# Optimization experiments

Hardware: AMD Instinct MI355X
Metric: run time of the kernel (lower is better)

The kernel has to match this reference:

```python
import jax, jax.numpy as jnp
import numpy as np
from functools import lru_cache
from jax.scipy.linalg import expm

N_QUBITS = 6
DIM = 2 ** N_QUBITS          # 64
N_PAULI = 4 ** N_QUBITS      # 4096


@lru_cache(maxsize=None)
def _pauli_tensor_np(n_qubits):
    # All n-qubit Pauli strings as dense matrices, ordered base-4
    # (digit 0..3 -> I, X, Y, Z; most-significant digit = first qubit).
    I = np.eye(2, dtype=np.complex64)
    X = np.array([[0, 1], [1, 0]], dtype=np.complex64)
    Y = np.array([[0, -1j], [1j, 0]], dtype=np.complex64)
    Z = np.array([[1, 0], [0, -1]], dtype=np.complex64)
    base = np.stack([I, X, Y, Z])  # [4,2,2]
    T = base
    for _ in range(n_qubits - 1):
        k, d = T.shape[0], T.shape[1]
        T = np.einsum('iab,jcd->ijacbd', T, base).reshape(k * 4, d * 2, d * 2)
    return np.ascontiguousarray(T.astype(np.complex64))  # [4^n, 2^n, 2^n]


def setup_inputs() -> dict:
    key = jax.random.key(0)
    kx, kw, kb = jax.random.split(key, 3)
    x = jax.random.normal(kx, (512, 4000), dtype=jnp.float32)
    weight = jax.random.normal(kw, (4, N_PAULI - 1), dtype=jnp.float32)
    bias = jax.random.normal(kb, (DIM,), dtype=jnp.float32)
    return {"x": x, "weight": weight, "bias": bias}


def reference(x, weight, bias):
    # x: [B, in_dim] float32; weight: [n_reps, 4^n - 1]; bias: [out_dim]
    B, in_dim = x.shape
    n_reps = weight.shape[0]
    out_dim = bias.shape[0]
    P = jnp.asarray(_pauli_tensor_np(N_QUBITS))  # [4096, 64, 64] complex64

    # Pad data coefficients up to the full Pauli basis (identity included).
    xp = jnp.pad(x, ((0, 0), (0, N_PAULI - in_dim))).astype(jnp.complex64)

    # Data-encoding Hamiltonian per sample: H_d[b] = sum_p x[b,p] * P[p]
    Hd = jnp.einsum('bp,pij->bij', xp, P)                       # [B,64,64]
    Ud = jax.vmap(expm)(-1j * Hd)                               # [B,64,64]

    # Trainable Hamiltonians per rep (identity Pauli excluded -> global phase).
    Hp = jnp.einsum('rp,pij->rij', weight.astype(jnp.complex64), P[1:])
    Up = jax.vmap(expm)(-1j * Hp)                               # [R,64,64]

    # Data re-uploading circuit on |0...0>: repeat (U_param @ U_data).
    psi = jnp.zeros((B, DIM), dtype=jnp.complex64).at[:, 0].set(1.0)
    for r in range(n_reps):
        psi = jnp.einsum('bij,bj->bi', Ud, psi)
        psi = jnp.einsum('ij,bj->bi', Up[r], psi)

    # Observables are computational-basis projectors |k><k|, k < out_dim:
    # <psi|O_k|psi> = |psi_k|^2
    probs = (psi[:, :out_dim].real ** 2 + psi[:, :out_dim].imag ** 2)
    return probs.astype(jnp.float32) + bias
```

## Files before the change

kernel.cpp:

```cpp
#include <hip/hip_runtime.h>
#include <math.h>

typedef float2 cplx;
typedef __attribute__((ext_vector_type(8))) short short8v;
typedef __attribute__((ext_vector_type(4))) short short4v;
typedef __attribute__((ext_vector_type(4))) float float4v;

#define IN_DIM 4000
#define NREPS 4

#define C0f  1.0f
#define C1f  1.0f
#define C2f  0.5f
#define C3f  0.16666667f
#define C4f  0.041666668f
#define C5f  8.3333333e-3f
#define C6f  1.3888889e-3f
#define C7f  1.9841270e-4f
#define C8f  2.4801587e-5f
#define C9f  2.7557319e-6f
#define C10f 2.7557319e-7f
#define C11f 2.5052108e-8f
#define C12f 2.0876757e-9f
#define C13f 1.6059044e-10f
#define C14f 1.1470746e-11f
#define C15f 7.6471637e-13f

#define MFMA(A,B,C) __builtin_amdgcn_mfma_f32_16x16x32_bf16((A),(B),(C),0,0,0)


__device__ __forceinline__ int idxSw(int a, int b) {
    return (a << 6) + ((((b >> 3) + a) & 7) << 3) + (b & 7);
}
__device__ __forceinline__ short f2bf(float f) {
    unsigned u = __float_as_uint(f);
    return (short)((u + 0x7FFF + ((u >> 16) & 1)) >> 16);
}
__device__ __forceinline__ float bf2f(short s) {
    return __uint_as_float(((unsigned)(unsigned short)s) << 16);
}
__device__ __forceinline__ short8v neg8(short8v a) {
    int4 u; __builtin_memcpy(&u, &a, 16);
    u.x ^= 0x80008000; u.y ^= 0x80008000; u.z ^= 0x80008000; u.w ^= 0x80008000;
    short8v r; __builtin_memcpy(&r, &u, 16); return r;
}

template<int AM, int BM, int NDM, int NDN>
__device__ __forceinline__ void mm_mfma(const short* __restrict__ As,
                                        const short* __restrict__ Bs,
                                        int li, int q, int mb, int nb,
                                        float4v* __restrict__ accR,
                                        float4v* __restrict__ accI)
{
    #pragma unroll
    for (int ks = 0; ks < 2; ks++) {
        const int ch = ks * 4 + q;
        short8v arh[NDM], arl[NDM], cRh[NDM], cRl[NDM], cIh[NDM], cIl[NDM];
        #pragma unroll
        for (int dm = 0; dm < NDM; dm++) {
            int r = ((mb + dm) << 4) + li;
            int off = (r << 6) + (((ch + r) & 7) << 3);
            arh[dm] = *(const short8v*)(As + off);
            arl[dm] = *(const short8v*)(As + 4096 + off);
            short8v aih = *(const short8v*)(As + 8192 + off);
            short8v ail = *(const short8v*)(As + 12288 + off);
            short8v nih = neg8(aih), nil_ = neg8(ail);
            cRh[dm] = (AM == 2) ? aih : nih;
            cRl[dm] = (AM == 2) ? ail : nil_;
            cIh[dm] = (AM == 2) ? nih : aih;
            cIl[dm] = (AM == 2) ? nil_ : ail;
        }
        #pragma unroll
        for (int dn = 0; dn < NDN; dn++) {
            int n = ((nb + dn) << 4) + li;
            int off = (n << 6) + (((ch + n) & 7) << 3);
            short8v brh = *(const short8v*)(Bs + off);
            short8v brl = *(const short8v*)(Bs + 4096 + off);
            short8v bih = *(const short8v*)(Bs + 8192 + off);
            short8v bil = *(const short8v*)(Bs + 12288 + off);
            if (BM == 1) { brh = neg8(brh); brl = neg8(brl); }
            __builtin_amdgcn_s_setprio(1);
            #pragma unroll
            for (int dm = 0; dm < NDM; dm++) {
                int ti = dm * NDN + dn;
                accR[ti] = MFMA(arh[dm], brh, accR[ti]);
                accR[ti] = MFMA(arh[dm], brl, accR[ti]);
                accR[ti] = MFMA(arl[dm], brh, accR[ti]);
                accR[ti] = MFMA(cRh[dm], bih, accR[ti]);
                accR[ti] = MFMA(cRh[dm], bil, accR[ti]);
                accR[ti] = MFMA(cRl[dm], bih, accR[ti]);
                accI[ti] = MFMA(arh[dm], bih, accI[ti]);
                accI[ti] = MFMA(arh[dm], bil, accI[ti]);
                accI[ti] = MFMA(arl[dm], bih, accI[ti]);
                accI[ti] = MFMA(cIh[dm], brh, accI[ti]);
                accI[ti] = MFMA(cIh[dm], brl, accI[ti]);
                accI[ti] = MFMA(cIl[dm], brh, accI[ti]);
            }
            __builtin_amdgcn_s_setprio(0);
        }
    }
}

template<int NDM, int NDN>
__device__ __forceinline__ void write_row(short* __restrict__ S, int li, int q,
                                          int mb, int nb,
                                          const float4v* cre, const float4v* cim)
{
    #pragma unroll
    for (int dm = 0; dm < NDM; dm++)
    #pragma unroll
    for (int dn = 0; dn < NDN; dn++) {
        int ti = dm * NDN + dn;
        int c = ((nb + dn) << 4) + li;
        #pragma unroll
        for (int reg = 0; reg < 4; reg++) {
            int r = ((mb + dm) << 4) + q * 4 + reg;
            int off = idxSw(r, c);
            float vr = cre[ti][reg], vi = cim[ti][reg];
            short rh = f2bf(vr), rl = f2bf(vr - bf2f(rh));
            short ih = f2bf(vi), il = f2bf(vi - bf2f(ih));
            S[off] = rh; S[4096 + off] = rl; S[8192 + off] = ih; S[12288 + off] = il;
        }
    }
}

template<int NDM, int NDN>
__device__ __forceinline__ void write_rowT(short* __restrict__ S, int li, int q,
                                           int mb, int nb,
                                           const float4v* cre, const float4v* cim)
{
    #pragma unroll
    for (int dm = 0; dm < NDM; dm++)
    #pragma unroll
    for (int dn = 0; dn < NDN; dn++) {
        int ti = dm * NDN + dn;
        int c = ((nb + dn) << 4) + li;
        int k0 = ((mb + dm) << 4) + q * 4;
        int off = idxSw(c, k0);
        short4v rh, rl, ih, il;
        #pragma unroll
        for (int reg = 0; reg < 4; reg++) {
            float vr = cre[ti][reg], vi = cim[ti][reg];
            short h1 = f2bf(vr); rh[reg] = h1; rl[reg] = f2bf(vr - bf2f(h1));
            short h2 = f2bf(vi); ih[reg] = h2; il[reg] = f2bf(vi - bf2f(h2));
        }
        *(short4v*)(S + off) = rh;
        *(short4v*)(S + 4096 + off) = rl;
        *(short4v*)(S + 8192 + off) = ih;
        *(short4v*)(S + 12288 + off) = il;
    }
}

template<int NDM, int NDN>
__device__ __forceinline__ void gather_tile(const short* __restrict__ S, int li, int q,
                                            int mb, int nb, float4v* bre, float4v* bim)
{
    #pragma unroll
    for (int dm = 0; dm < NDM; dm++)
    #pragma unroll
    for (int dn = 0; dn < NDN; dn++) {
        int ti = dm * NDN + dn;
        int c = ((nb + dn) << 4) + li;
        #pragma unroll
        for (int reg = 0; reg < 4; reg++) {
            int r = ((mb + dm) << 4) + q * 4 + reg;
            int off = idxSw(r, c);
            bre[ti][reg] = bf2f(S[off]) + bf2f(S[4096 + off]);
            bim[ti][reg] = bf2f(S[8192 + off]) + bf2f(S[12288 + off]);
        }
    }
}

template<int NDM, int NDN>
__device__ __forceinline__ void adddiag(float4v* u, float cI, int li, int q, int mb, int nb)
{
    #pragma unroll
    for (int dm = 0; dm < NDM; dm++)
    #pragma unroll
    for (int dn = 0; dn < NDN; dn++) {
        if (mb + dm == nb + dn) {
            #pragma unroll
            for (int e = 0; e < 4; e++)
                if (li == q * 4 + e) u[dm * NDN + dn][e] += cI;
        }
    }
}

template<int NDM, int NDN>
__device__ __forceinline__ void store_tiles(cplx* __restrict__ dst, int li, int q,
                                            int mb, int nb,
                                            const float4v* ure, const float4v* uim)
{
    #pragma unroll
    for (int dm = 0; dm < NDM; dm++)
    #pragma unroll
    for (int dn = 0; dn < NDN; dn++) {
        int ti = dm * NDN + dn;
        int c = ((nb + dn) << 4) + li;
        int cs = c ^ (((c >> 4) & 1) << 1);
        #pragma unroll
        for (int reg = 0; reg < 4; reg++) {
            int r = ((mb + dm) << 4) + q * 4 + reg;
            dst[(r << 6) + cs] = make_float2(ure[ti][reg], uim[ti][reg]);
        }
    }
}

__device__ __forceinline__ cplx pauli_phase(float v, int xm, int zm) {
    int ny = __popc(xm & zm) & 3;
    if (ny == 0) return make_float2(v, 0.f);
    if (ny == 1) return make_float2(0.f, -v);
    if (ny == 2) return make_float2(-v, 0.f);
    return make_float2(0.f, v);
}

__device__ __forceinline__ void expm_core8(char* __restrict__ LDS,
                                           const float* __restrict__ src, bool isW,
                                           int t, float4v* ure, float4v* uim)
{
    constexpr int NDM = 1, NDN = 2, NT = 2;
    short* S0 = (short*)LDS;
    short* S1 = (short*)(LDS + 32768);
    cplx*  W  = (cplx*)(LDS + 32768);
    float* red = (float*)(LDS + 65536);
    const int lane = t & 63, wv = t >> 6;
    const int li = lane & 15, q = lane >> 4;
    const int mb = wv & 3, nb = (wv >> 2) << 1;

    float sumsq = 0.f;
    #pragma unroll
    for (int n = 0; n < 8; n++) {
        int p = t + 512 * n;
        int xm = 0, zm = 0;
        #pragma unroll
        for (int k = 0; k < 6; k++) {
            int d = (p >> (2 * k)) & 3;
            int hi = d >> 1, lo = d & 1;
            zm |= hi << k; xm |= (hi ^ lo) << k;
        }
        float v = isW ? ((p == 0) ? 0.f : src[p - 1])
                      : ((p < IN_DIM) ? src[p] : 0.f);
        sumsq += v * v;
        W[(xm << 6) + zm] = pauli_phase(v, xm, zm);
    }
    #pragma unroll
    for (int d = 32; d >= 1; d >>= 1) sumsq += __shfl_xor(sumsq, d, 64);
    if (lane == 0) red[wv] = sumsq;
    __syncthreads();

    float rs = 0.f;
    #pragma unroll
    for (int i2 = 0; i2 < 8; i2++) rs += red[i2];
    float fro = sqrtf(64.f * rs);
    int s1 = 0; { float nn = fro; while (nn > 8.f && s1 < 24) { nn *= 0.5f; s1++; } }
    float sc1 = exp2f((float)(-s1));

    cplx hv[8];
    #pragma unroll
    for (int rr = 0; rr < 8; rr++) hv[rr] = W[((wv * 8 + rr) << 6) + lane];
    #pragma unroll
    for (int d = 1; d < 64; d <<= 1) {
        float sg = (lane & d) ? -1.f : 1.f;
        #pragma unroll
        for (int rr = 0; rr < 8; rr++) {
            float px = __shfl_xor(hv[rr].x, d, 64);
            float py = __shfl_xor(hv[rr].y, d, 64);
            hv[rr].x = fmaf(sg, hv[rr].x, px);
            hv[rr].y = fmaf(sg, hv[rr].y, py);
        }
    }

    #pragma unroll
    for (int rr = 0; rr < 8; rr++) {
        int m = wv * 8 + rr;
        int c = lane ^ m;
        float vr = hv[rr].y * sc1, vi = -hv[rr].x * sc1;
        short rh = f2bf(vr), rl = f2bf(vr - bf2f(rh));
        short ih = f2bf(vi), il = f2bf(vi - bf2f(ih));
        int off = idxSw(lane, c);
        S0[off] = rh; S0[4096 + off] = rl; S0[8192 + off] = ih; S0[12288 + off] = il;
    }
    __syncthreads();

    const float4v z4 = {0.f, 0.f, 0.f, 0.f};
    float4v accR[NT], accI[NT];
    #define ZERO_ACC _Pragma("unroll") for (int i2 = 0; i2 < NT; i2++) { accR[i2]=z4; accI[i2]=z4; }

    ZERO_ACC
    mm_mfma<0, 1, NDM, NDN>(S0, S0, li, q, mb, nb, accR, accI);
    float ss = 0.f;
    #pragma unroll
    for (int ti = 0; ti < NT; ti++)
        #pragma unroll
        for (int e = 0; e < 4; e++)
            ss += accR[ti][e]*accR[ti][e] + accI[ti][e]*accI[ti][e];
    #pragma unroll
    for (int d = 32; d >= 1; d >>= 1) ss += __shfl_xor(ss, d, 64);
    if (lane == 0) red[8 + wv] = ss;
    __syncthreads();

    rs = 0.f;
    #pragma unroll
    for (int i2 = 0; i2 < 8; i2++) rs += red[8 + i2];
    float bound = sqrtf(sqrtf(rs));
    int ds = 0; { float nn = bound; while (nn > 3.4f && ds < 12) { nn *= 0.5f; ds++; } }
    const int s = s1 + ds;
    float dsc = exp2f((float)(-ds)), dsc2 = dsc * dsc;

    float4v bre[NT], bim[NT];
    gather_tile<NDM, NDN>(S0, li, q, mb, nb, bre, bim);

    #pragma unroll
    for (int ti = 0; ti < NT; ti++) { ure[ti] = accR[ti] * dsc2; uim[ti] = accI[ti] * dsc2; }
    write_rowT<NDM, NDN>(S1, li, q, mb, nb, ure, uim);
    __syncthreads();

    {
        float ca = C15f * dsc;
        #pragma unroll
        for (int ti = 0; ti < NT; ti++) { ure[ti] = ca * bre[ti]; uim[ti] = ca * bim[ti]; }
        adddiag<NDM, NDN>(ure, C14f, li, q, mb, nb);
        write_rowT<NDM, NDN>(S0, li, q, mb, nb, ure, uim);
    }
    __syncthreads();

    const float cIc[7] = { C0f, C2f, C4f, C6f, C8f, C10f, C12f };
    const float cAc[7] = { C1f, C3f, C5f, C7f, C9f, C11f, C13f };
    for (int j = 6; j >= 0; j--) {
        ZERO_ACC
        mm_mfma<2, 0, NDM, NDN>(S1, S0, li, q, mb, nb, accR, accI);
        __syncthreads();
        float ca = cAc[j] * dsc, cI = cIc[j];
        #pragma unroll
        for (int ti = 0; ti < NT; ti++) {
            ure[ti] = accR[ti] + ca * bre[ti];
            uim[ti] = accI[ti] + ca * bim[ti];
        }
        adddiag<NDM, NDN>(ure, cI, li, q, mb, nb);
        write_rowT<NDM, NDN>(S0, li, q, mb, nb, ure, uim);
        __syncthreads();
    }

    for (int sq = 0; sq < s; sq++) {
        write_row<NDM, NDN>(S1, li, q, mb, nb, ure, uim);
        if (sq > 0) write_rowT<NDM, NDN>(S0, li, q, mb, nb, ure, uim);
        __syncthreads();
        ZERO_ACC
        mm_mfma<0, 0, NDM, NDN>(S1, S0, li, q, mb, nb, accR, accI);
        __syncthreads();
        #pragma unroll
        for (int ti = 0; ti < NT; ti++) { ure[ti] = accR[ti]; uim[ti] = accI[ti]; }
    }
    #undef ZERO_ACC
}

__device__ __forceinline__ cplx matvec_wave8(const cplx* __restrict__ M,
                                             const cplx* __restrict__ pin,
                                             int lane, int wv)
{
    const int ri = lane & 7;
    const int rr = (wv << 3) + ri;
    const int kc = lane >> 3;
    const int ch = (kc + ri) & 7;
    const int b  = (ch >> 1) & 1;
    const float4* Mr = (const float4*)(M + (rr << 6)) + (ch << 2);
    float4 m0 = Mr[0 ^ b], m1 = Mr[1 ^ b], m2 = Mr[2 ^ b], m3 = Mr[3 ^ b];
    const cplx* p = pin + (ch << 3);
    cplx p0 = p[0], p1 = p[1], p2 = p[2], p3 = p[3];
    cplx p4 = p[4], p5 = p[5], p6 = p[6], p7 = p[7];
    float ax = 0.f, ay = 0.f;
    ax = fmaf(m0.x, p0.x, fmaf(-m0.y, p0.y, ax));
    ay = fmaf(m0.x, p0.y, fmaf( m0.y, p0.x, ay));
    ax = fmaf(m0.z, p1.x, fmaf(-m0.w, p1.y, ax));
    ay = fmaf(m0.z, p1.y, fmaf( m0.w, p1.x, ay));
    ax = fmaf(m1.x, p2.x, fmaf(-m1.y, p2.y, ax));
    ay = fmaf(m1.x, p2.y, fmaf( m1.y, p2.x, ay));
    ax = fmaf(m1.z, p3.x, fmaf(-m1.w, p3.y, ax));
    ay = fmaf(m1.z, p3.y, fmaf( m1.w, p3.x, ay));
    ax = fmaf(m2.x, p4.x, fmaf(-m2.y, p4.y, ax));
    ay = fmaf(m2.x, p4.y, fmaf( m2.y, p4.x, ay));
    ax = fmaf(m2.z, p5.x, fmaf(-m2.w, p5.y, ax));
    ay = fmaf(m2.z, p5.y, fmaf( m2.w, p5.x, ay));
    ax = fmaf(m3.x, p6.x, fmaf(-m3.y, p6.y, ax));
    ay = fmaf(m3.x, p6.y, fmaf( m3.y, p6.x, ay));
    ax = fmaf(m3.z, p7.x, fmaf(-m3.w, p7.y, ax));
    ay = fmaf(m3.z, p7.y, fmaf( m3.w, p7.x, ay));
    ax += __shfl_xor(ax, 8, 64);  ay += __shfl_xor(ay, 8, 64);
    ax += __shfl_xor(ax, 16, 64); ay += __shfl_xor(ay, 16, 64);
    ax += __shfl_xor(ax, 32, 64); ay += __shfl_xor(ay, 32, 64);
    return make_float2(ax, ay);
}

__global__ __launch_bounds__(512, 2) void circuit_kernel(const float* __restrict__ x,
                                                         const float* __restrict__ w,
                                                         const float* __restrict__ bias,
                                                         cplx* __restrict__ ws,
                                                         int* __restrict__ flag,
                                                         float* __restrict__ out)
{
    __shared__ float4 LDSf4[4168];
    char* LDS = (char*)LDSf4;
    const int t = threadIdx.x, b = blockIdx.x;
    const int lane = t & 63, wv = t >> 6, li = lane & 15, q = lane >> 4;
    const int mb = wv & 3, nb = (wv >> 2) << 1;
    float4v ure[2], uim[2];

    for (int duty = (b < NREPS) ? 0 : 1; duty < 2; duty++) {
        const bool isW = (duty == 0);
        const float* src = isW ? (w + (size_t)b * 4095) : (x + (size_t)b * IN_DIM);
        expm_core8(LDS, src, isW, t, ure, uim);
        if (isW) {
            store_tiles<1, 2>(ws + ((size_t)b << 12), li, q, mb, nb, ure, uim);
            __syncthreads();
            if (t == 0)
                __hip_atomic_fetch_add(flag, 1, __ATOMIC_RELEASE, __HIP_MEMORY_SCOPE_AGENT);
        }
    }

    cplx* Ud   = (cplx*)(LDS + 32768);
    cplx* UpS  = (cplx*)LDS;
    cplx* psiA = (cplx*)(LDS + 65664);
    cplx* psiB = (cplx*)(LDS + 66176);

    store_tiles<1, 2>(Ud, li, q, mb, nb, ure, uim);
    if (t < 64) psiA[t] = make_float2(t == 0 ? 1.f : 0.f, 0.f);
    if (t == 0) {
        while (__hip_atomic_load(flag, __ATOMIC_ACQUIRE, __HIP_MEMORY_SCOPE_AGENT) < NREPS)
            __builtin_amdgcn_s_sleep(8);
    }
    __syncthreads();

    const int rowi = (wv << 3) + (lane & 7);
    for (int r = 0; r < NREPS; r++) {
        {
            const float4* srcv = (const float4*)(ws + ((size_t)r << 12));
            float4* dstY = (float4*)UpS;
            #pragma unroll
            for (int n = 0; n < 4; n++) dstY[n * 512 + t] = srcv[n * 512 + t];
        }
        cplx v1 = matvec_wave8(Ud, psiA, lane, wv);
        if (lane < 8) psiB[rowi] = v1;
        __syncthreads();
        cplx v2 = matvec_wave8(UpS, psiB, lane, wv);
        if (lane < 8) psiA[rowi] = v2;
        __syncthreads();
    }
    if (t < 64) {
        cplx pv = psiA[t];
        out[(b << 6) + t] = fmaf(pv.x, pv.x, fmaf(pv.y, pv.y, bias[t]));
    }
}

extern "C" void kernel_launch(void* const* d_in, const int* in_sizes, int n_in,
                              void* d_out, int out_size, void* d_ws, size_t ws_size,
                              hipStream_t stream)
{
    const float* x    = (const float*)d_in[0];
    const float* w    = (const float*)d_in[1];
    const float* bias = (const float*)d_in[2];
    float* out = (float*)d_out;
    cplx* ws   = (cplx*)d_ws;
    int* flag  = (int*)((char*)d_ws + (NREPS << 15));

    int B = in_sizes[0] / IN_DIM;

    hipMemsetAsync(flag, 0, sizeof(int), stream);
    hipLaunchKernelGGL(circuit_kernel, dim3(B), dim3(512), 0, stream,
                       x, w, bias, ws, flag, out);
}
```

Measured before the change: 175.2 us.

## Use 1024-thread blocks with one MFMA tile per wave and double-buffered LDS

Doubles the block to 16 waves so each wave computes a single 16x16 complex tile instead of two, and grows LDS to 128KB with four split-bf16 buffers. The Horner loop ping-pongs between two buffers to drop one barrier per step, and squaring alternates buffer pairs. The matvec is re-partitioned across 16 waves. In exchange, only one block fits per CU (previously two of 512 threads), and the larger LDS footprint lowers occupancy across the 512 independent blocks.

```diff
diff --git a/kernel.cpp b/kernel.cpp
--- a/kernel.cpp
+++ b/kernel.cpp
@@ -45,7 +45,7 @@
     short8v r; __builtin_memcpy(&r, &u, 16); return r;
 }
 
-template<int AM, int BM, int NDM, int NDN>
+template<int AM, int BM>
 __device__ __forceinline__ void mm_mfma(const short* __restrict__ As,
                                         const short* __restrict__ Bs,
                                         int li, int q, int mb, int nb,
@@ -55,154 +55,109 @@
     #pragma unroll
     for (int ks = 0; ks < 2; ks++) {
         const int ch = ks * 4 + q;
-        short8v arh[NDM], arl[NDM], cRh[NDM], cRl[NDM], cIh[NDM], cIl[NDM];
-        #pragma unroll
-        for (int dm = 0; dm < NDM; dm++) {
-            int r = ((mb + dm) << 4) + li;
-            int off = (r << 6) + (((ch + r) & 7) << 3);
-            arh[dm] = *(const short8v*)(As + off);
-            arl[dm] = *(const short8v*)(As + 4096 + off);
-            short8v aih = *(const short8v*)(As + 8192 + off);
-            short8v ail = *(const short8v*)(As + 12288 + off);
-            short8v nih = neg8(aih), nil_ = neg8(ail);
-            cRh[dm] = (AM == 2) ? aih : nih;
-            cRl[dm] = (AM == 2) ? ail : nil_;
-            cIh[dm] = (AM == 2) ? nih : aih;
-            cIl[dm] = (AM == 2) ? nil_ : ail;
-        }
-        #pragma unroll
-        for (int dn = 0; dn < NDN; dn++) {
-            int n = ((nb + dn) << 4) + li;
-            int off = (n << 6) + (((ch + n) & 7) << 3);
-            short8v brh = *(const short8v*)(Bs + off);
-            short8v brl = *(const short8v*)(Bs + 4096 + off);
-            short8v bih = *(const short8v*)(Bs + 8192 + off);
-            short8v bil = *(const short8v*)(Bs + 12288 + off);
-            if (BM == 1) { brh = neg8(brh); brl = neg8(brl); }
-            __builtin_amdgcn_s_setprio(1);
-            #pragma unroll
-            for (int dm = 0; dm < NDM; dm++) {
-                int ti = dm * NDN + dn;
-                accR[ti] = MFMA(arh[dm], brh, accR[ti]);
-                accR[ti] = MFMA(arh[dm], brl, accR[ti]);
-                accR[ti] = MFMA(arl[dm], brh, accR[ti]);
-                accR[ti] = MFMA(cRh[dm], bih, accR[ti]);
-                accR[ti] = MFMA(cRh[dm], bil, accR[ti]);
-                accR[ti] = MFMA(cRl[dm], bih, accR[ti]);
-                accI[ti] = MFMA(arh[dm], bih, accI[ti]);
-                accI[ti] = MFMA(arh[dm], bil, accI[ti]);
-                accI[ti] = MFMA(arl[dm], bih, accI[ti]);
-                accI[ti] = MFMA(cIh[dm], brh, accI[ti]);
-                accI[ti] = MFMA(cIh[dm], brl, accI[ti]);
-                accI[ti] = MFMA(cIl[dm], brh, accI[ti]);
-            }
-            __builtin_amdgcn_s_setprio(0);
-        }
-    }
-}
-
-template<int NDM, int NDN>
-__device__ __forceinline__ void write_row(short* __restrict__ S, int li, int q,
-                                          int mb, int nb,
-                                          const float4v* cre, const float4v* cim)
-{
-    #pragma unroll
-    for (int dm = 0; dm < NDM; dm++)
-    #pragma unroll
-    for (int dn = 0; dn < NDN; dn++) {
-        int ti = dm * NDN + dn;
-        int c = ((nb + dn) << 4) + li;
-        #pragma unroll
-        for (int reg = 0; reg < 4; reg++) {
-            int r = ((mb + dm) << 4) + q * 4 + reg;
-            int off = idxSw(r, c);
-            float vr = cre[ti][reg], vi = cim[ti][reg];
-            short rh = f2bf(vr), rl = f2bf(vr - bf2f(rh));
-            short ih = f2bf(vi), il = f2bf(vi - bf2f(ih));
-            S[off] = rh; S[4096 + off] = rl; S[8192 + off] = ih; S[12288 + off] = il;
-        }
-    }
-}
-
-template<int NDM, int NDN>
-__device__ __forceinline__ void write_rowT(short* __restrict__ S, int li, int q,
+        int r = (mb << 4) + li;
+        int offA = (r << 6) + (((ch + r) & 7) << 3);
+        short8v arh = *(const short8v*)(As + offA);
+        short8v arl = *(const short8v*)(As + 4096 + offA);
+        short8v aih = *(const short8v*)(As + 8192 + offA);
+        short8v ail = *(const short8v*)(As + 12288 + offA);
+        short8v nih = neg8(aih), nil_ = neg8(ail);
+        short8v cRh = (AM == 2) ? aih : nih;
+        short8v cRl = (AM == 2) ? ail : nil_;
+        short8v cIh = (AM == 2) ? nih : aih;
+        short8v cIl = (AM == 2) ? nil_ : ail;
+
+        int n = (nb << 4) + li;
+        int offB = (n << 6) + (((ch + n) & 7) << 3);
+        short8v brh = *(const short8v*)(Bs + offB);
+        short8v brl = *(const short8v*)(Bs + 4096 + offB);
+        short8v bih = *(const short8v*)(Bs + 8192 + offB);
+        short8v bil = *(const short8v*)(Bs + 12288 + offB);
+        if (BM == 1) { brh = neg8(brh); brl = neg8(brl); }
+
+        accR[0] = MFMA(arh, brh, accR[0]);
+        accR[0] = MFMA(arh, brl, accR[0]);
+        accR[0] = MFMA(arl, brh, accR[0]);
+        accR[0] = MFMA(cRh, bih, accR[0]);
+        accR[0] = MFMA(cRh, bil, accR[0]);
+        accR[0] = MFMA(cRl, bih, accR[0]);
+        accI[0] = MFMA(arh, bih, accI[0]);
+        accI[0] = MFMA(arh, bil, accI[0]);
+        accI[0] = MFMA(arl, bih, accI[0]);
+        accI[0] = MFMA(cIh, brh, accI[0]);
+        accI[0] = MFMA(cIh, brl, accI[0]);
+        accI[0] = MFMA(cIl, brh, accI[0]);
+    }
+}
+
+__device__ __forceinline__ void write_row1(short* __restrict__ S, int li, int q,
                                            int mb, int nb,
                                            const float4v* cre, const float4v* cim)
 {
-    #pragma unroll
-    for (int dm = 0; dm < NDM; dm++)
-    #pragma unroll
-    for (int dn = 0; dn < NDN; dn++) {
-        int ti = dm * NDN + dn;
-        int c = ((nb + dn) << 4) + li;
-        int k0 = ((mb + dm) << 4) + q * 4;
-        int off = idxSw(c, k0);
-        short4v rh, rl, ih, il;
+    int c = (nb << 4) + li;
+    #pragma unroll
+    for (int reg = 0; reg < 4; reg++) {
+        int r = (mb << 4) + q * 4 + reg;
+        int off = idxSw(r, c);
+        float vr = cre[0][reg], vi = cim[0][reg];
+        short rh = f2bf(vr), rl = f2bf(vr - bf2f(rh));
+        short ih = f2bf(vi), il = f2bf(vi - bf2f(ih));
+        S[off] = rh; S[4096 + off] = rl; S[8192 + off] = ih; S[12288 + off] = il;
+    }
+}
+
+__device__ __forceinline__ void write_rowT1(short* __restrict__ S, int li, int q,
+                                            int mb, int nb,
+                                            const float4v* cre, const float4v* cim)
+{
+    int c = (nb << 4) + li;
+    int k0 = (mb << 4) + q * 4;
+    int off = idxSw(c, k0);
+    short4v rh, rl, ih, il;
+    #pragma unroll
+    for (int reg = 0; reg < 4; reg++) {
+        float vr = cre[0][reg], vi = cim[0][reg];
+        short h1 = f2bf(vr); rh[reg] = h1; rl[reg] = f2bf(vr - bf2f(h1));
+        short h2 = f2bf(vi); ih[reg] = h2; il[reg] = f2bf(vi - bf2f(h2));
+    }
+    *(short4v*)(S + off) = rh;
+    *(short4v*)(S + 4096 + off) = rl;
+    *(short4v*)(S + 8192 + off) = ih;
+    *(short4v*)(S + 12288 + off) = il;
+}
+
+__device__ __forceinline__ void gather_tile1(const short* __restrict__ S, int li, int q,
+                                             int mb, int nb, float4v* bre, float4v* bim)
+{
+    int c = (nb << 4) + li;
+    #pragma unroll
+    for (int reg = 0; reg < 4; reg++) {
+        int r = (mb << 4) + q * 4 + reg;
+        int off = idxSw(r, c);
+        bre[0][reg] = bf2f(S[off]) + bf2f(S[4096 + off]);
+        bim[0][reg] = bf2f(S[8192 + off]) + bf2f(S[12288 + off]);
+    }
+}
+
+__device__ __forceinline__ void adddiag1(float4v* u, float cI, int li, int q, int mb, int nb)
+{
+    if (mb == nb) {
         #pragma unroll
-        for (int reg = 0; reg < 4; reg++) {
-            float vr = cre[ti][reg], vi = cim[ti][reg];
-            short h1 = f2bf(vr); rh[reg] = h1; rl[reg] = f2bf(vr - bf2f(h1));
-            short h2 = f2bf(vi); ih[reg] = h2; il[reg] = f2bf(vi - bf2f(h2));
-        }
-        *(short4v*)(S + off) = rh;
-        *(short4v*)(S + 4096 + off) = rl;
-        *(short4v*)(S + 8192 + off) = ih;
-        *(short4v*)(S + 12288 + off) = il;
-    }
-}
-
-template<int NDM, int NDN>
-__device__ __forceinline__ void gather_tile(const short* __restrict__ S, int li, int q,
-                                            int mb, int nb, float4v* bre, float4v* bim)
-{
-    #pragma unroll
-    for (int dm = 0; dm < NDM; dm++)
-    #pragma unroll
-    for (int dn = 0; dn < NDN; dn++) {
-        int ti = dm * NDN + dn;
-        int c = ((nb + dn) << 4) + li;
-        #pragma unroll
-        for (int reg = 0; reg < 4; reg++) {
-            int r = ((mb + dm) << 4) + q * 4 + reg;
-            int off = idxSw(r, c);
-            bre[ti][reg] = bf2f(S[off]) + bf2f(S[4096 + off]);
-            bim[ti][reg] = bf2f(S[8192 + off]) + bf2f(S[12288 + off]);
-        }
-    }
-}
-
-template<int NDM, int NDN>
-__device__ __forceinline__ void adddiag(float4v* u, float cI, int li, int q, int mb, int nb)
-{
-    #pragma unroll
-    for (int dm = 0; dm < NDM; dm++)
-    #pragma unroll
-    for (int dn = 0; dn < NDN; dn++) {
-        if (mb + dm == nb + dn) {
-            #pragma unroll
-            for (int e = 0; e < 4; e++)
-                if (li == q * 4 + e) u[dm * NDN + dn][e] += cI;
-        }
-    }
-}
-
-template<int NDM, int NDN>
-__device__ __forceinline__ void store_tiles(cplx* __restrict__ dst, int li, int q,
-                                            int mb, int nb,
-                                            const float4v* ure, const float4v* uim)
-{
-    #pragma unroll
-    for (int dm = 0; dm < NDM; dm++)
-    #pragma unroll
-    for (int dn = 0; dn < NDN; dn++) {
-        int ti = dm * NDN + dn;
-        int c = ((nb + dn) << 4) + li;
-        int cs = c ^ (((c >> 4) & 1) << 1);
-        #pragma unroll
-        for (int reg = 0; reg < 4; reg++) {
-            int r = ((mb + dm) << 4) + q * 4 + reg;
-            dst[(r << 6) + cs] = make_float2(ure[ti][reg], uim[ti][reg]);
-        }
+        for (int e = 0; e < 4; e++)
+            if (li == q * 4 + e) u[0][e] += cI;
+    }
+}
+
+__device__ __forceinline__ void store_tiles1(cplx* __restrict__ dst, int li, int q,
+                                             int mb, int nb,
+                                             const float4v* ure, const float4v* uim)
+{
+    int c = (nb << 4) + li;
+    int cs = c ^ (((c >> 4) & 1) << 1);
+    #pragma unroll
+    for (int reg = 0; reg < 4; reg++) {
+        int r = (mb << 4) + q * 4 + reg;
+        dst[(r << 6) + cs] = make_float2(ure[0][reg], uim[0][reg]);
     }
 }
 
@@ -214,23 +169,24 @@
     return make_float2(0.f, v);
 }
 
-__device__ __forceinline__ void expm_core8(char* __restrict__ LDS,
-                                           const float* __restrict__ src, bool isW,
-                                           int t, float4v* ure, float4v* uim)
-{
-    constexpr int NDM = 1, NDN = 2, NT = 2;
-    short* S0 = (short*)LDS;
-    short* S1 = (short*)(LDS + 32768);
-    cplx*  W  = (cplx*)(LDS + 32768);
-    float* red = (float*)(LDS + 65536);
+__device__ __forceinline__ void expm_core16(char* __restrict__ LDS,
+                                            const float* __restrict__ src, bool isW,
+                                            int t, float4v* ure, float4v* uim)
+{
+    short* P0 = (short*)LDS;
+    short* P1 = (short*)(LDS + 32768);
+    short* P2 = (short*)(LDS + 65536);
+    short* P3 = (short*)(LDS + 98304);
+    cplx*  W  = (cplx*)(LDS + 65536);
+    float* red = (float*)(LDS + 98304);
     const int lane = t & 63, wv = t >> 6;
     const int li = lane & 15, q = lane >> 4;
-    const int mb = wv & 3, nb = (wv >> 2) << 1;
+    const int mb = wv & 3, nb = wv >> 2;
 
     float sumsq = 0.f;
     #pragma unroll
-    for (int n = 0; n < 8; n++) {
-        int p = t + 512 * n;
+    for (int n = 0; n < 4; n++) {
+        int p = t + 1024 * n;
         int xm = 0, zm = 0;
         #pragma unroll
         for (int k = 0; k < 6; k++) {
@@ -250,124 +206,116 @@
 
     float rs = 0.f;
     #pragma unroll
-    for (int i2 = 0; i2 < 8; i2++) rs += red[i2];
+    for (int i2 = 0; i2 < 16; i2++) rs += red[i2];
     float fro = sqrtf(64.f * rs);
     int s1 = 0; { float nn = fro; while (nn > 8.f && s1 < 24) { nn *= 0.5f; s1++; } }
     float sc1 = exp2f((float)(-s1));
 
-    cplx hv[8];
-    #pragma unroll
-    for (int rr = 0; rr < 8; rr++) hv[rr] = W[((wv * 8 + rr) << 6) + lane];
+    cplx hv[4];
+    #pragma unroll
+    for (int rr = 0; rr < 4; rr++) hv[rr] = W[((wv * 4 + rr) << 6) + lane];
     #pragma unroll
     for (int d = 1; d < 64; d <<= 1) {
         float sg = (lane & d) ? -1.f : 1.f;
         #pragma unroll
-        for (int rr = 0; rr < 8; rr++) {
+        for (int rr = 0; rr < 4; rr++) {
             float px = __shfl_xor(hv[rr].x, d, 64);
             float py = __shfl_xor(hv[rr].y, d, 64);
             hv[rr].x = fmaf(sg, hv[rr].x, px);
             hv[rr].y = fmaf(sg, hv[rr].y, py);
         }
     }
-
-    #pragma unroll
-    for (int rr = 0; rr < 8; rr++) {
-        int m = wv * 8 + rr;
+    #pragma unroll
+    for (int rr = 0; rr < 4; rr++) {
+        int m = wv * 4 + rr;
         int c = lane ^ m;
         float vr = hv[rr].y * sc1, vi = -hv[rr].x * sc1;
         short rh = f2bf(vr), rl = f2bf(vr - bf2f(rh));
         short ih = f2bf(vi), il = f2bf(vi - bf2f(ih));
         int off = idxSw(lane, c);
-        S0[off] = rh; S0[4096 + off] = rl; S0[8192 + off] = ih; S0[12288 + off] = il;
+        P0[off] = rh; P0[4096 + off] = rl; P0[8192 + off] = ih; P0[12288 + off] = il;
     }
     __syncthreads();
 
     const float4v z4 = {0.f, 0.f, 0.f, 0.f};
-    float4v accR[NT], accI[NT];
-    #define ZERO_ACC _Pragma("unroll") for (int i2 = 0; i2 < NT; i2++) { accR[i2]=z4; accI[i2]=z4; }
+    float4v accR[1], accI[1];
+    #define ZERO_ACC { accR[0] = z4; accI[0] = z4; }
 
     ZERO_ACC
-    mm_mfma<0, 1, NDM, NDN>(S0, S0, li, q, mb, nb, accR, accI);
+    mm_mfma<0, 1>(P0, P0, li, q, mb, nb, accR, accI);
+    write_rowT1(P1, li, q, mb, nb, accR, accI);
     float ss = 0.f;
     #pragma unroll
-    for (int ti = 0; ti < NT; ti++)
-        #pragma unroll
-        for (int e = 0; e < 4; e++)
-            ss += accR[ti][e]*accR[ti][e] + accI[ti][e]*accI[ti][e];
+    for (int e = 0; e < 4; e++)
+        ss += accR[0][e]*accR[0][e] + accI[0][e]*accI[0][e];
     #pragma unroll
     for (int d = 32; d >= 1; d >>= 1) ss += __shfl_xor(ss, d, 64);
-    if (lane == 0) red[8 + wv] = ss;
+    if (lane == 0) red[16 + wv] = ss;
     __syncthreads();
 
     rs = 0.f;
     #pragma unroll
-    for (int i2 = 0; i2 < 8; i2++) rs += red[8 + i2];
+    for (int i2 = 0; i2 < 16; i2++) rs += red[16 + i2];
     float bound = sqrtf(sqrtf(rs));
     int ds = 0; { float nn = bound; while (nn > 3.4f && ds < 12) { nn *= 0.5f; ds++; } }
     const int s = s1 + ds;
     float dsc = exp2f((float)(-ds)), dsc2 = dsc * dsc;
 
-    float4v bre[NT], bim[NT];
-    gather_tile<NDM, NDN>(S0, li, q, mb, nb, bre, bim);
-
-    #pragma unroll
-    for (int ti = 0; ti < NT; ti++) { ure[ti] = accR[ti] * dsc2; uim[ti] = accI[ti] * dsc2; }
-    write_rowT<NDM, NDN>(S1, li, q, mb, nb, ure, uim);
-    __syncthreads();
+    float4v bre[1], bim[1];
+    gather_tile1(P0, li, q, mb, nb, bre, bim);
 
     {
         float ca = C15f * dsc;
-        #pragma unroll
-        for (int ti = 0; ti < NT; ti++) { ure[ti] = ca * bre[ti]; uim[ti] = ca * bim[ti]; }
-        adddiag<NDM, NDN>(ure, C14f, li, q, mb, nb);
-        write_rowT<NDM, NDN>(S0, li, q, mb, nb, ure, uim);
+        ure[0] = ca * bre[0]; uim[0] = ca * bim[0];
+        adddiag1(ure, C14f, li, q, mb, nb);
+        write_rowT1(P2, li, q, mb, nb, ure, uim);
     }
     __syncthreads();
 
     const float cIc[7] = { C0f, C2f, C4f, C6f, C8f, C10f, C12f };
     const float cAc[7] = { C1f, C3f, C5f, C7f, C9f, C11f, C13f };
+    short* Vr = P2; short* Vw = P3;
     for (int j = 6; j >= 0; j--) {
         ZERO_ACC
-        mm_mfma<2, 0, NDM, NDN>(S1, S0, li, q, mb, nb, accR, accI);
+        mm_mfma<2, 0>(P1, Vr, li, q, mb, nb, accR, accI);
+        float ca = cAc[j] * dsc, cI = cIc[j];
+        ure[0] = dsc2 * accR[0] + ca * bre[0];
+        uim[0] = dsc2 * accI[0] + ca * bim[0];
+        adddiag1(ure, cI, li, q, mb, nb);
+        if (j > 0) {
+            write_rowT1(Vw, li, q, mb, nb, ure, uim);
+            short* tmp = Vr; Vr = Vw; Vw = tmp;
+        }
         __syncthreads();
-        float ca = cAc[j] * dsc, cI = cIc[j];
-        #pragma unroll
-        for (int ti = 0; ti < NT; ti++) {
-            ure[ti] = accR[ti] + ca * bre[ti];
-            uim[ti] = accI[ti] + ca * bim[ti];
-        }
-        adddiag<NDM, NDN>(ure, cI, li, q, mb, nb);
-        write_rowT<NDM, NDN>(S0, li, q, mb, nb, ure, uim);
-        __syncthreads();
     }
 
     for (int sq = 0; sq < s; sq++) {
-        write_row<NDM, NDN>(S1, li, q, mb, nb, ure, uim);
-        if (sq > 0) write_rowT<NDM, NDN>(S0, li, q, mb, nb, ure, uim);
+        short* Ua = (sq & 1) ? P2 : P0;
+        short* Ub = (sq & 1) ? P3 : P1;
+        write_row1(Ua, li, q, mb, nb, ure, uim);
+        write_rowT1(Ub, li, q, mb, nb, ure, uim);
         __syncthreads();
         ZERO_ACC
-        mm_mfma<0, 0, NDM, NDN>(S1, S0, li, q, mb, nb, accR, accI);
+        mm_mfma<0, 0>(Ua, Ub, li, q, mb, nb, accR, accI);
         __syncthreads();
-        #pragma unroll
-        for (int ti = 0; ti < NT; ti++) { ure[ti] = accR[ti]; uim[ti] = accI[ti]; }
+        ure[0] = accR[0]; uim[0] = accI[0];
     }
     #undef ZERO_ACC
 }
 
-__device__ __forceinline__ cplx matvec_wave8(const cplx* __restrict__ M,
-                                             const cplx* __restrict__ pin,
-                                             int lane, int wv)
-{
-    const int ri = lane & 7;
-    const int rr = (wv << 3) + ri;
-    const int kc = lane >> 3;
-    const int ch = (kc + ri) & 7;
-    const int b  = (ch >> 1) & 1;
-    const float4* Mr = (const float4*)(M + (rr << 6)) + (ch << 2);
-    float4 m0 = Mr[0 ^ b], m1 = Mr[1 ^ b], m2 = Mr[2 ^ b], m3 = Mr[3 ^ b];
-    const cplx* p = pin + (ch << 3);
+__device__ __forceinline__ cplx matvec_wave16(const cplx* __restrict__ M,
+                                              const cplx* __restrict__ pin,
+                                              int lane, int wv)
+{
+    const int ri = lane & 3;
+    const int rr = (wv << 2) + ri;
+    const int kc = lane >> 2;
+    const int ch = (kc + rr) & 15;
+    const int b  = (ch >> 2) & 1;
+    const float4* Mr = (const float4*)(M + (rr << 6)) + (ch << 1);
+    float4 m0 = Mr[b], m1 = Mr[1 - b];
+    const cplx* p = pin + (ch << 2);
     cplx p0 = p[0], p1 = p[1], p2 = p[2], p3 = p[3];
-    cplx p4 = p[4], p5 = p[5], p6 = p[6], p7 = p[7];
     float ax = 0.f, ay = 0.f;
     ax = fmaf(m0.x, p0.x, fmaf(-m0.y, p0.y, ax));
     ay = fmaf(m0.x, p0.y, fmaf( m0.y, p0.x, ay));
@@ -377,52 +325,45 @@
     ay = fmaf(m1.x, p2.y, fmaf( m1.y, p2.x, ay));
     ax = fmaf(m1.z, p3.x, fmaf(-m1.w, p3.y, ax));
     ay = fmaf(m1.z, p3.y, fmaf( m1.w, p3.x, ay));
-    ax = fmaf(m2.x, p4.x, fmaf(-m2.y, p4.y, ax));
-    ay = fmaf(m2.x, p4.y, fmaf( m2.y, p4.x, ay));
-    ax = fmaf(m2.z, p5.x, fmaf(-m2.w, p5.y, ax));
-    ay = fmaf(m2.z, p5.y, fmaf( m2.w, p5.x, ay));
-    ax = fmaf(m3.x, p6.x, fmaf(-m3.y, p6.y, ax));
-    ay = fmaf(m3.x, p6.y, fmaf( m3.y, p6.x, ay));
-    ax = fmaf(m3.z, p7.x, fmaf(-m3.w, p7.y, ax));
-    ay = fmaf(m3.z, p7.y, fmaf( m3.w, p7.x, ay));
+    ax += __shfl_xor(ax, 4, 64);  ay += __shfl_xor(ay, 4, 64);
     ax += __shfl_xor(ax, 8, 64);  ay += __shfl_xor(ay, 8, 64);
     ax += __shfl_xor(ax, 16, 64); ay += __shfl_xor(ay, 16, 64);
     ax += __shfl_xor(ax, 32, 64); ay += __shfl_xor(ay, 32, 64);
     return make_float2(ax, ay);
 }
 
-__global__ __launch_bounds__(512, 2) void circuit_kernel(const float* __restrict__ x,
-                                                         const float* __restrict__ w,
-                                                         const float* __restrict__ bias,
-                                                         cplx* __restrict__ ws,
-                                                         int* __restrict__ flag,
-                                                         float* __restrict__ out)
-{
-    __shared__ float4 LDSf4[4168];
+__global__ __launch_bounds__(1024) void circuit_kernel(const float* __restrict__ x,
+                                                       const float* __restrict__ w,
+                                                       const float* __restrict__ bias,
+                                                       cplx* __restrict__ ws,
+                                                       int* __restrict__ flag,
+                                                       float* __restrict__ out)
+{
+    __shared__ float4 LDSf4[8192];
     char* LDS = (char*)LDSf4;
     const int t = threadIdx.x, b = blockIdx.x;
     const int lane = t & 63, wv = t >> 6, li = lane & 15, q = lane >> 4;
-    const int mb = wv & 3, nb = (wv >> 2) << 1;
-    float4v ure[2], uim[2];
+    const int mb = wv & 3, nb = wv >> 2;
+    float4v ure[1], uim[1];
 
     for (int duty = (b < NREPS) ? 0 : 1; duty < 2; duty++) {
         const bool isW = (duty == 0);
         const float* src = isW ? (w + (size_t)b * 4095) : (x + (size_t)b * IN_DIM);
-        expm_core8(LDS, src, isW, t, ure, uim);
+        expm_core16(LDS, src, isW, t, ure, uim);
         if (isW) {
-            store_tiles<1, 2>(ws + ((size_t)b << 12), li, q, mb, nb, ure, uim);
+            store_tiles1(ws + ((size_t)b << 12), li, q, mb, nb, ure, uim);
             __syncthreads();
             if (t == 0)
                 __hip_atomic_fetch_add(flag, 1, __ATOMIC_RELEASE, __HIP_MEMORY_SCOPE_AGENT);
         }
     }
 
-    cplx* Ud   = (cplx*)(LDS + 32768);
-    cplx* UpS  = (cplx*)LDS;
-    cplx* psiA = (cplx*)(LDS + 65664);
-    cplx* psiB = (cplx*)(LDS + 66176);
-
-    store_tiles<1, 2>(Ud, li, q, mb, nb, ure, uim);
+    cplx* Ud   = (cplx*)LDS;
+    cplx* UpS  = (cplx*)(LDS + 32768);
+    cplx* psiA = (cplx*)(LDS + 65536);
+    cplx* psiB = (cplx*)(LDS + 66048);
+
+    store_tiles1(Ud, li, q, mb, nb, ure, uim);
     if (t < 64) psiA[t] = make_float2(t == 0 ? 1.f : 0.f, 0.f);
     if (t == 0) {
         while (__hip_atomic_load(flag, __ATOMIC_ACQUIRE, __HIP_MEMORY_SCOPE_AGENT) < NREPS)
@@ -430,19 +371,19 @@
     }
     __syncthreads();
 
-    const int rowi = (wv << 3) + (lane & 7);
+    const int rowi = (wv << 2) + (lane & 3);
     for (int r = 0; r < NREPS; r++) {
         {
             const float4* srcv = (const float4*)(ws + ((size_t)r << 12));
             float4* dstY = (float4*)UpS;
-            #pragma unroll
-            for (int n = 0; n < 4; n++) dstY[n * 512 + t] = srcv[n * 512 + t];
+            dstY[t] = srcv[t];
+            dstY[1024 + t] = srcv[1024 + t];
         }
-        cplx v1 = matvec_wave8(Ud, psiA, lane, wv);
-        if (lane < 8) psiB[rowi] = v1;
+        cplx v1 = matvec_wave16(Ud, psiA, lane, wv);
+        if (lane < 4) psiB[rowi] = v1;
         __syncthreads();
-        cplx v2 = matvec_wave8(UpS, psiB, lane, wv);
-        if (lane < 8) psiA[rowi] = v2;
+        cplx v2 = matvec_wave16(UpS, psiB, lane, wv);
+        if (lane < 4) psiA[rowi] = v2;
         __syncthreads();
     }
     if (t < 64) {
@@ -465,6 +406,6 @@
     int B = in_sizes[0] / IN_DIM;
 
     hipMemsetAsync(flag, 0, sizeof(int), stream);
-    hipLaunchKernelGGL(circuit_kernel, dim3(B), dim3(512), 0, stream,
+    hipLaunchKernelGGL(circuit_kernel, dim3(B), dim3(1024), 0, stream,
                        x, w, bias, ws, flag, out);
 }
```

New measurement: 163.5 us. 6.7% less time.
